# Optimization experiments

Measured on AMD Instinct MI355X. Metric: run time of the kernel, lower is better.

Reference implementation:

```python
import jax, jax.numpy as jnp
import numpy as np

QUANT_RANGE = 2688.0  # 6 (max E2M1) * 448 (max E4M3), tllm static_6 rule
EPS = 1e-12
BLOCK = 16  # NVFP4 block size along K


def _round_e2m1(v):
    # Round to the E2M1 grid {0, .5, 1, 1.5, 2, 3, 4, 6} (signed), RTNE on the grid.
    a = jnp.abs(v)
    # quantization step doubles with the exponent: 0.5 for |a|<2, 1 for [2,4), 2 for [4,6]
    e = jnp.floor(jnp.log2(jnp.maximum(a, 1e-30)))
    step = jnp.exp2(jnp.maximum(e, 0.0) - 1.0)
    q = jnp.minimum(jnp.round(a / step) * step, 6.0)
    return jnp.sign(v) * q


def _round_e4m3(v):
    # FP8 E4M3 round-trip (block scale factors are stored as E4M3)
    return v.astype(jnp.float8_e4m3fn).astype(jnp.float32)


def _fp4_quantize(t2d, global_scale):
    # t2d: [R, K] -> (e2m1 codes [R, K/16, 16], e4m3 block scales [R, K/16])
    R, K = t2d.shape
    tb = t2d.reshape(R, K // BLOCK, BLOCK)
    block_amax = jnp.max(jnp.abs(tb), axis=-1)            # [R, K/16]
    sf = _round_e4m3(block_amax * global_scale / 6.0)      # FP8 scale per block
    sf_safe = jnp.maximum(sf, EPS)
    q = _round_e2m1(tb * (global_scale / sf_safe)[..., None])
    return q, sf


def _nvfp4_linear(x, weight, bias):
    in_features = weight.shape[1]
    out_features = weight.shape[0]
    orig_shape = x.shape
    x2 = x.reshape(-1, in_features)                        # [M, K]
    M = x2.shape[0]

    # weight quantization (done once at from_linear time in the original)
    w_amax = jnp.maximum(jnp.max(jnp.abs(weight)), EPS)
    w_gs = QUANT_RANGE / w_amax
    qw, sfw = _fp4_quantize(weight, w_gs)                  # [N, K/16, 16], [N, K/16]

    # dynamic activation quantization
    a_amax = jnp.maximum(jnp.max(jnp.abs(x2)), EPS)
    a_gs = QUANT_RANGE / a_amax
    qx, sfx = _fp4_quantize(x2, a_gs)                      # [M, K/16, 16], [M, K/16]

    # alpha = act_amax * (weight_amax / quant_range^2)
    alpha = a_amax * w_amax / (QUANT_RANGE * QUANT_RANGE)

    # block-scaled GEMM: out[m,n] = alpha * sum_b sfx[m,b] sfw[n,b] (qx[m,b,:] . qw[n,b,:])
    # fused as a dense GEMM over per-block-scaled codes (mathematically identical)
    dx = (qx * sfx[..., None]).reshape(M, in_features)
    dw = (qw * sfw[..., None]).reshape(out_features, in_features)
    out = alpha * (dx @ dw.T) + bias
    return out.reshape(*orig_shape[:-1], out_features)


def setup_inputs() -> dict:
    key = jax.random.key(0)
    k1, k2, k3 = jax.random.split(key, 3)
    x = jax.random.normal(k1, (2, 2048, 4096), dtype=jnp.float32)
    weight = jax.random.normal(k2, (4096, 4096), dtype=jnp.float32) * 0.02
    bias = jax.random.normal(k3, (4096,), dtype=jnp.float32) * 0.01
    return {"x": x, "weight": weight, "bias": bias}


def reference(x, weight, bias):
    return _nvfp4_linear(x, weight, bias)
```

## Files before the change

kernel.cpp:

```cpp
#include <hip/hip_runtime.h>
#include <hip/hip_bf16.h>


typedef unsigned short u16;
typedef __bf16 bf16x8 __attribute__((ext_vector_type(8)));
typedef float f32x4 __attribute__((ext_vector_type(4)));
typedef unsigned short u16x8 __attribute__((ext_vector_type(8)));

#define GLD_LDS(gsrc, ldst)                                                     \
  __builtin_amdgcn_global_load_lds(                                             \
      (const __attribute__((address_space(1))) void*)(gsrc),                    \
      (__attribute__((address_space(3))) void*)(ldst), 16, 0, 0)

#define SBAR()                                                                  \
  do {                                                                          \
    asm volatile("" ::: "memory");                                              \
    __builtin_amdgcn_s_barrier();                                               \
    asm volatile("" ::: "memory");                                              \
  } while (0)

#define VMCNT_(N) asm volatile("s_waitcnt vmcnt(" #N ")" ::: "memory")
#define VMCNT(N) VMCNT_(N)


__device__ __forceinline__ float round_e4m3(float v) {
  if (v < 0.015625f) {
    return rintf(v * 512.0f) * 0.001953125f;
  }
  unsigned b = __float_as_uint(v);
  unsigned e = (b >> 23) & 0xFFu;
  float step = __uint_as_float((e - 3u) << 23);
  return rintf(v / step) * step;
}

__device__ __forceinline__ float round_e2m1(float v) {
  float a = fabsf(v);
  float step = (a < 2.0f) ? 0.5f : ((a < 4.0f) ? 1.0f : 2.0f);
  float q = fminf(rintf(a / step) * step, 6.0f);
  return copysignf(q, v);
}


__global__ void nvfp4_amax_kernel(const float* __restrict__ x,
                                  const float* __restrict__ w,
                                  unsigned* __restrict__ sc, int nx4, int nw4) {
  const float4* src = blockIdx.y ? (const float4*)w : (const float4*)x;
  int n4 = blockIdx.y ? nw4 : nx4;
  float m = 0.f;
  for (int i = blockIdx.x * blockDim.x + threadIdx.x; i < n4;
       i += gridDim.x * blockDim.x) {
    float4 v = src[i];
    m = fmaxf(m, fmaxf(fmaxf(fabsf(v.x), fabsf(v.y)),
                       fmaxf(fabsf(v.z), fabsf(v.w))));
  }
#pragma unroll
  for (int off = 32; off; off >>= 1) m = fmaxf(m, __shfl_down(m, off));
  __shared__ float red[4];
  if ((threadIdx.x & 63) == 0) red[threadIdx.x >> 6] = m;
  __syncthreads();
  if (threadIdx.x == 0) {
    m = fmaxf(fmaxf(red[0], red[1]), fmaxf(red[2], red[3]));
    atomicMax(&sc[blockIdx.y], __float_as_uint(m));
  }
}


__global__ void nvfp4_quant_kernel(const float* __restrict__ src,
                                   u16* __restrict__ dst,
                                   const unsigned* __restrict__ sc, int which,
                                   int nblk) {
  int idx = blockIdx.x * blockDim.x + threadIdx.x;
  if (idx >= nblk) return;
  float amax = fmaxf(__uint_as_float(sc[which]), 1e-12f);
  float gs = 2688.0f / amax;

  float4 v[4];
  const float4* p = (const float4*)src + (size_t)idx * 4;
  v[0] = p[0]; v[1] = p[1]; v[2] = p[2]; v[3] = p[3];
  const float* fv = (const float*)v;

  float bamax = 0.f;
#pragma unroll
  for (int i = 0; i < 16; ++i) bamax = fmaxf(bamax, fabsf(fv[i]));

  float sf = round_e4m3((bamax * gs) / 6.0f);
  float sfs = fmaxf(sf, 1e-12f);
  float r = gs / sfs;

  u16 ob[16];
#pragma unroll
  for (int i = 0; i < 16; ++i) {
    float q = round_e2m1(fv[i] * r);
    float d = q * sf;
    ob[i] = (u16)(__float_as_uint(d) >> 16);
  }
  u16x8* o = (u16x8*)(dst + (size_t)idx * 16);
  o[0] = *(u16x8*)ob;
  o[1] = *(u16x8*)(ob + 8);
}


#define BM 256
#define BN 256
#define BK 32
#define TILE_E 8192

__global__ __launch_bounds__(512, 2) void nvfp4_gemm_kernel(
    const u16* __restrict__ A,
    const u16* __restrict__ B,
    const float* __restrict__ bias, const unsigned* __restrict__ sc,
    float* __restrict__ C, int M, int N, int K) {
  __shared__ u16 lA[4][TILE_E];
  __shared__ u16 lB[4][TILE_E];
  const u16* lAflat = &lA[0][0];
  const u16* lBflat = &lB[0][0];

  const int tid = threadIdx.x;
  const int lane = tid & 63;
  const int wv = tid >> 6;
  const int wm = wv >> 2;
  const int wn = wv & 3;

  const int bid = blockIdx.x;
  const int xcd = bid & 7, loc = bid >> 3;
  const int tm0 = ((xcd & 3) * 4 + (loc & 3)) * BM;
  const int tn0 = ((xcd >> 2) * 8 + (loc >> 2)) * BN;

  const int srow = tid >> 2;
  const int skey = (srow >> 1) & 3;
  const int scol = ((tid & 3) ^ skey) * 8;
  const u16* gA0 = A + (size_t)(tm0 + srow) * K + scol;
  const u16* gA1 = A + (size_t)(tm0 + 128 + srow) * K + scol;
  const u16* gB0 = B + (size_t)(tn0 + srow) * K + scol;
  const u16* gB1 = B + (size_t)(tn0 + 128 + srow) * K + scol;
  const int ld0 = tid * 8;
  const int ld1 = tid * 8 + 4096;

#define STAGE_A(tt)                                                             \
  do {                                                                          \
    int _o = ((tt) & 3) * TILE_E;                                               \
    GLD_LDS(gA0 + (size_t)(tt) * BK, lAflat + _o + ld0);                        \
    GLD_LDS(gA1 + (size_t)(tt) * BK, lAflat + _o + ld1);                        \
  } while (0)
#define STAGE_B(tt)                                                             \
  do {                                                                          \
    int _o = ((tt) & 3) * TILE_E;                                               \
    GLD_LDS(gB0 + (size_t)(tt) * BK, lBflat + _o + ld0);                        \
    GLD_LDS(gB1 + (size_t)(tt) * BK, lBflat + _o + ld1);                        \
  } while (0)

  const int rb = lane & 15;
  const int cc = (((lane >> 4) ^ ((rb >> 1) & 3)) << 3);
  const int aoff = (wm * 128 + rb) * BK + cc;
  const int boff = (wn * 64 + rb) * BK + cc;

#define READ_AB(AV, BV, tt)                                                     \
  do {                                                                          \
    const u16* _ba = lAflat + ((tt) & 3) * TILE_E;                              \
    const u16* _bb = lBflat + ((tt) & 3) * TILE_E;                              \
    AV[0] = *(const bf16x8*)(_ba + aoff);                                       \
    AV[1] = *(const bf16x8*)(_ba + aoff + 512);                                 \
    AV[2] = *(const bf16x8*)(_ba + aoff + 1024);                                \
    AV[3] = *(const bf16x8*)(_ba + aoff + 1536);                                \
    BV[0] = *(const bf16x8*)(_bb + boff);                                       \
    BV[1] = *(const bf16x8*)(_bb + boff + 512);                                 \
    BV[2] = *(const bf16x8*)(_bb + boff + 1024);                                \
    BV[3] = *(const bf16x8*)(_bb + boff + 1536);                                \
  } while (0)

#define READ_AW(AW, tt)                                                         \
  do {                                                                          \
    const u16* _ba = lAflat + ((tt) & 3) * TILE_E + 2048;         \
    AW[0] = *(const bf16x8*)(_ba + aoff);                                       \
    AW[1] = *(const bf16x8*)(_ba + aoff + 512);                                 \
    AW[2] = *(const bf16x8*)(_ba + aoff + 1024);                                \
    AW[3] = *(const bf16x8*)(_ba + aoff + 1536);                                \
  } while (0)

#define MFMA_IH0(AV, BV)                                                        \
  do {                                                                          \
    _Pragma("unroll") for (int _i = 0; _i < 4; ++_i)                            \
        _Pragma("unroll") for (int _j = 0; _j < 4; ++_j)                        \
            acc[_i][_j] = __builtin_amdgcn_mfma_f32_16x16x32_bf16(              \
                AV[_i], BV[_j], acc[_i][_j], 0, 0, 0);                          \
  } while (0)

#define MFMA_IH1(AW, BV)                                                        \
  do {                                                                          \
    _Pragma("unroll") for (int _i = 0; _i < 4; ++_i)                            \
        _Pragma("unroll") for (int _j = 0; _j < 4; ++_j)                        \
            acc[4 + _i][_j] = __builtin_amdgcn_mfma_f32_16x16x32_bf16(          \
                AW[_i], BV[_j], acc[4 + _i][_j], 0, 0, 0);                      \
  } while (0)

#define TILE_STEP(CAV, CBV, CAW, NAV, NBV, t, VM, STA, STB, RDN)                \
  do {                                                                          \
    if (STA) STAGE_A((t) + 3);                                                  \
    VMCNT(VM);                                                                  \
    SBAR();                                                                     \
    READ_AW(CAW, t);                                                            \
    __builtin_amdgcn_s_setprio(1);                                              \
    MFMA_IH0(CAV, CBV);                                                         \
    __builtin_amdgcn_s_setprio(0);                                              \
    if (STB) STAGE_B((t) + 3);                                                  \
    if (RDN) READ_AB(NAV, NBV, (t) + 1);                                        \
    __builtin_amdgcn_s_setprio(1);                                              \
    MFMA_IH1(CAW, CBV);                                                         \
    __builtin_amdgcn_s_setprio(0);                                              \
    SBAR();                                                                     \
  } while (0)

  f32x4 acc[8][4] = {};
  bf16x8 xav[4], xbv[4], xaw[4], yav[4], ybv[4], yaw[4];

  STAGE_A(0); STAGE_B(0);
  STAGE_A(1); STAGE_B(1);
  STAGE_A(2); STAGE_B(2);
  VMCNT(4);
  SBAR();
  READ_AB(xav, xbv, 0);

  for (int p = 0; p < 62; ++p) {
    const int t0 = 2 * p;
    TILE_STEP(xav, xbv, xaw, yav, ybv, t0,     6, 1, 1, 1);
    TILE_STEP(yav, ybv, yaw, xav, xbv, t0 + 1, 6, 1, 1, 1);
  }
  TILE_STEP(xav, xbv, xaw, yav, ybv, 124, 6, 1, 1, 1);
  TILE_STEP(yav, ybv, yaw, xav, xbv, 125, 4, 0, 0, 1);
  TILE_STEP(xav, xbv, xaw, yav, ybv, 126, 0, 0, 0, 1);
  TILE_STEP(yav, ybv, yaw, xav, xbv, 127, 0, 0, 0, 0);

  float ax = fmaxf(__uint_as_float(sc[0]), 1e-12f);
  float aw_ = fmaxf(__uint_as_float(sc[1]), 1e-12f);
  float alpha = (ax * aw_) / 7225344.0f;

  const int orow = (lane >> 4) * 4;
  const int ocol = lane & 15;
#pragma unroll
  for (int ai = 0; ai < 8; ++ai) {
#pragma unroll
    for (int j = 0; j < 4; ++j) {
      int col = tn0 + wn * 64 + j * 16 + ocol;
      float bvv = bias[col];
#pragma unroll
      for (int rr = 0; rr < 4; ++rr) {
        int row = tm0 + wm * 128 + ai * 16 + orow + rr;
        C[(size_t)row * N + col] = alpha * acc[ai][j][rr] + bvv;
      }
    }
  }
#undef STAGE_A
#undef STAGE_B
#undef READ_AB
#undef READ_AW
#undef MFMA_IH0
#undef MFMA_IH1
#undef TILE_STEP
}


extern "C" void kernel_launch(void* const* d_in, const int* in_sizes, int n_in,
                              void* d_out, int out_size, void* d_ws, size_t ws_size,
                              hipStream_t stream) {
  const float* x = (const float*)d_in[0];
  const float* w = (const float*)d_in[1];
  const float* bias = (const float*)d_in[2];
  float* out = (float*)d_out;

  const int N = in_sizes[2];
  const int K = in_sizes[1] / N;
  const int M = in_sizes[0] / K;

  unsigned char* ws = (unsigned char*)d_ws;
  unsigned* sc = (unsigned*)ws;
  u16* dx = (u16*)(ws + 256);
  u16* dw = (u16*)(ws + 256 + (size_t)M * K * sizeof(u16));

  hipMemsetAsync(sc, 0, 8, stream);

  nvfp4_amax_kernel<<<dim3(256, 2), 256, 0, stream>>>(x, w, sc, M * K / 4,
                                                      N * K / 4);

  int nbx = M * K / 16, nbw = N * K / 16;
  nvfp4_quant_kernel<<<(nbx + 255) / 256, 256, 0, stream>>>(x, dx, sc, 0, nbx);
  nvfp4_quant_kernel<<<(nbw + 255) / 256, 256, 0, stream>>>(w, dw, sc, 1, nbw);

  nvfp4_gemm_kernel<<<dim3((M / BM) * (N / BN)), 512, 0, stream>>>(
      dx, dw, bias, sc, out, M, N, K);
}
```

Measured before the change: 197.0 us.

## Drop register double-buffering of LDS fragments, load all per tile; widen amax grid

The GEMM main loop stops prefetching the next tile's A/B fragments from LDS into a second register set during the current MFMAs. Each tile step now loads all 12 fragments after the barrier and then runs the 32 MFMAs in row order, with VMCNT thresholds recomputed for the simpler loop. This frees registers, which could improve occupancy or scheduling, at the cost of exposing LDS read latency at the start of each tile. Separately, the amax reduction kernel launches four times as many blocks to use more of the GPU.

```diff
diff --git a/kernel.cpp b/kernel.cpp
--- a/kernel.cpp
+++ b/kernel.cpp
@@ -154,81 +154,61 @@
   const int aoff = (wm * 128 + rb) * BK + cc;
   const int boff = (wn * 64 + rb) * BK + cc;
 
-#define READ_AB(AV, BV, tt)                                                     \
-  do {                                                                          \
-    const u16* _ba = lAflat + ((tt) & 3) * TILE_E;                              \
-    const u16* _bb = lBflat + ((tt) & 3) * TILE_E;                              \
-    AV[0] = *(const bf16x8*)(_ba + aoff);                                       \
-    AV[1] = *(const bf16x8*)(_ba + aoff + 512);                                 \
-    AV[2] = *(const bf16x8*)(_ba + aoff + 1024);                                \
-    AV[3] = *(const bf16x8*)(_ba + aoff + 1536);                                \
-    BV[0] = *(const bf16x8*)(_bb + boff);                                       \
-    BV[1] = *(const bf16x8*)(_bb + boff + 512);                                 \
-    BV[2] = *(const bf16x8*)(_bb + boff + 1024);                                \
-    BV[3] = *(const bf16x8*)(_bb + boff + 1536);                                \
-  } while (0)
-
-#define READ_AW(AW, tt)                                                         \
-  do {                                                                          \
-    const u16* _ba = lAflat + ((tt) & 3) * TILE_E + 2048;         \
-    AW[0] = *(const bf16x8*)(_ba + aoff);                                       \
-    AW[1] = *(const bf16x8*)(_ba + aoff + 512);                                 \
-    AW[2] = *(const bf16x8*)(_ba + aoff + 1024);                                \
-    AW[3] = *(const bf16x8*)(_ba + aoff + 1536);                                \
-  } while (0)
-
-#define MFMA_IH0(AV, BV)                                                        \
-  do {                                                                          \
-    _Pragma("unroll") for (int _i = 0; _i < 4; ++_i)                            \
-        _Pragma("unroll") for (int _j = 0; _j < 4; ++_j)                        \
-            acc[_i][_j] = __builtin_amdgcn_mfma_f32_16x16x32_bf16(              \
-                AV[_i], BV[_j], acc[_i][_j], 0, 0, 0);                          \
-  } while (0)
-
-#define MFMA_IH1(AW, BV)                                                        \
-  do {                                                                          \
-    _Pragma("unroll") for (int _i = 0; _i < 4; ++_i)                            \
-        _Pragma("unroll") for (int _j = 0; _j < 4; ++_j)                        \
-            acc[4 + _i][_j] = __builtin_amdgcn_mfma_f32_16x16x32_bf16(          \
-                AW[_i], BV[_j], acc[4 + _i][_j], 0, 0, 0);                      \
-  } while (0)
-
-#define TILE_STEP(CAV, CBV, CAW, NAV, NBV, t, VM, STA, STB, RDN)                \
+#define MFMA_ROW(r, AV)                                                         \
+  do {                                                                          \
+    acc[r][0] = __builtin_amdgcn_mfma_f32_16x16x32_bf16(AV, bv0, acc[r][0], 0, 0, 0); \
+    acc[r][1] = __builtin_amdgcn_mfma_f32_16x16x32_bf16(AV, bv1, acc[r][1], 0, 0, 0); \
+    acc[r][2] = __builtin_amdgcn_mfma_f32_16x16x32_bf16(AV, bv2, acc[r][2], 0, 0, 0); \
+    acc[r][3] = __builtin_amdgcn_mfma_f32_16x16x32_bf16(AV, bv3, acc[r][3], 0, 0, 0); \
+  } while (0)
+
+#define TILE_BODY(t, VM, STA, STB)                                              \
   do {                                                                          \
     if (STA) STAGE_A((t) + 3);                                                  \
     VMCNT(VM);                                                                  \
     SBAR();                                                                     \
-    READ_AW(CAW, t);                                                            \
+    const u16* _ba = lAflat + ((t) & 3) * TILE_E;                               \
+    const u16* _bb = lBflat + ((t) & 3) * TILE_E;                               \
+    bf16x8 bv0 = *(const bf16x8*)(_bb + boff);                                  \
+    bf16x8 bv1 = *(const bf16x8*)(_bb + boff + 512);                            \
+    bf16x8 bv2 = *(const bf16x8*)(_bb + boff + 1024);                           \
+    bf16x8 bv3 = *(const bf16x8*)(_bb + boff + 1536);                           \
+    bf16x8 av0 = *(const bf16x8*)(_ba + aoff);                                  \
+    bf16x8 av1 = *(const bf16x8*)(_ba + aoff + 512);                            \
+    bf16x8 av2 = *(const bf16x8*)(_ba + aoff + 1024);                           \
+    bf16x8 av3 = *(const bf16x8*)(_ba + aoff + 1536);                           \
+    bf16x8 aw0 = *(const bf16x8*)(_ba + aoff + 2048);                           \
+    bf16x8 aw1 = *(const bf16x8*)(_ba + aoff + 2560);                           \
+    bf16x8 aw2 = *(const bf16x8*)(_ba + aoff + 3072);                           \
+    bf16x8 aw3 = *(const bf16x8*)(_ba + aoff + 3584);                           \
     __builtin_amdgcn_s_setprio(1);                                              \
-    MFMA_IH0(CAV, CBV);                                                         \
+    MFMA_ROW(0, av0);                                                           \
+    MFMA_ROW(1, av1);                                                           \
     __builtin_amdgcn_s_setprio(0);                                              \
     if (STB) STAGE_B((t) + 3);                                                  \
-    if (RDN) READ_AB(NAV, NBV, (t) + 1);                                        \
     __builtin_amdgcn_s_setprio(1);                                              \
-    MFMA_IH1(CAW, CBV);                                                         \
+    MFMA_ROW(2, av2);                                                           \
+    MFMA_ROW(3, av3);                                                           \
+    MFMA_ROW(4, aw0);                                                           \
+    MFMA_ROW(5, aw1);                                                           \
+    MFMA_ROW(6, aw2);                                                           \
+    MFMA_ROW(7, aw3);                                                           \
     __builtin_amdgcn_s_setprio(0);                                              \
     SBAR();                                                                     \
   } while (0)
 
   f32x4 acc[8][4] = {};
-  bf16x8 xav[4], xbv[4], xaw[4], yav[4], ybv[4], yaw[4];
 
   STAGE_A(0); STAGE_B(0);
   STAGE_A(1); STAGE_B(1);
   STAGE_A(2); STAGE_B(2);
-  VMCNT(4);
-  SBAR();
-  READ_AB(xav, xbv, 0);
-
-  for (int p = 0; p < 62; ++p) {
-    const int t0 = 2 * p;
-    TILE_STEP(xav, xbv, xaw, yav, ybv, t0,     6, 1, 1, 1);
-    TILE_STEP(yav, ybv, yaw, xav, xbv, t0 + 1, 6, 1, 1, 1);
-  }
-  TILE_STEP(xav, xbv, xaw, yav, ybv, 124, 6, 1, 1, 1);
-  TILE_STEP(yav, ybv, yaw, xav, xbv, 125, 4, 0, 0, 1);
-  TILE_STEP(xav, xbv, xaw, yav, ybv, 126, 0, 0, 0, 1);
-  TILE_STEP(yav, ybv, yaw, xav, xbv, 127, 0, 0, 0, 0);
+
+  for (int t = 0; t < 125; ++t) {
+    TILE_BODY(t, 10, 1, 1);
+  }
+  TILE_BODY(125, 8, 0, 0);
+  TILE_BODY(126, 4, 0, 0);
+  TILE_BODY(127, 0, 0, 0);
 
   float ax = fmaxf(__uint_as_float(sc[0]), 1e-12f);
   float aw_ = fmaxf(__uint_as_float(sc[1]), 1e-12f);
@@ -251,11 +231,8 @@
   }
 #undef STAGE_A
 #undef STAGE_B
-#undef READ_AB
-#undef READ_AW
-#undef MFMA_IH0
-#undef MFMA_IH1
-#undef TILE_STEP
+#undef MFMA_ROW
+#undef TILE_BODY
 }
 
 
@@ -278,8 +255,8 @@
 
   hipMemsetAsync(sc, 0, 8, stream);
 
-  nvfp4_amax_kernel<<<dim3(256, 2), 256, 0, stream>>>(x, w, sc, M * K / 4,
-                                                      N * K / 4);
+  nvfp4_amax_kernel<<<dim3(1024, 2), 256, 0, stream>>>(x, w, sc, M * K / 4,
+                                                       N * K / 4);
 
   int nbx = M * K / 16, nbw = N * K / 16;
   nvfp4_quant_kernel<<<(nbx + 255) / 256, 256, 0, stream>>>(x, dx, sc, 0, nbx);
```

Result: slower. 212.7 us (+8.0%).
